# Optimization experiments

Hardware: AMD Instinct MI355X
Metric: run time of the kernel (lower is better)

The kernel has to match this reference:

```python
import jax, jax.numpy as jnp
import numpy as np

D_MODEL, D_K, D_V, H, M = 512, 64, 64, 8, 40
LN_EPS = 1e-3  # keras LayerNormalization default epsilon


def setup_inputs() -> dict:
    key = jax.random.key(0)
    ks = jax.random.split(key, 12)
    b, nq, nk = 16, 1024, 1024
    s = 1.0 / np.sqrt(D_MODEL)
    return {
        "queries": jax.random.normal(ks[0], (b, nq, D_MODEL), jnp.float32),
        "keys": jax.random.normal(ks[1], (b, nk, D_MODEL), jnp.float32),
        "values": jax.random.normal(ks[2], (b, nk, D_MODEL), jnp.float32),
        "attention_weights": jax.random.uniform(ks[3], (b, 1, nq, nk), jnp.float32),
        "Wq": jax.random.normal(ks[4], (D_MODEL, H * D_K), jnp.float32) * s,
        "bq": jnp.zeros((H * D_K,), jnp.float32),
        "Wk": jax.random.normal(ks[5], (D_MODEL, H * D_K), jnp.float32) * s,
        "bk": jnp.zeros((H * D_K,), jnp.float32),
        "Wv": jax.random.normal(ks[6], (D_MODEL, H * D_V), jnp.float32) * s,
        "bv": jnp.zeros((H * D_V,), jnp.float32),
        "Wo": jax.random.normal(ks[7], (H * D_V, D_MODEL), jnp.float32) * (1.0 / np.sqrt(H * D_V)),
        "bo": jnp.zeros((D_MODEL,), jnp.float32),
        "memK": jax.random.normal(ks[8], (1, M, H * D_K), jnp.float32) * (1.0 / D_K),
        "memV": jax.random.normal(ks[9], (1, M, H * D_V), jnp.float32) * (1.0 / M),
        "gamma": jnp.ones((D_MODEL,), jnp.float32),
        "beta": jnp.zeros((D_MODEL,), jnp.float32),
    }


def reference(queries, keys, values, attention_weights, Wq, bq, Wk, bk, Wv, bv,
              Wo, bo, memK, memV, gamma, beta):
    b, nq, _ = queries.shape
    nk = keys.shape[1]
    # scaled learned memory slots
    mem_k = np.sqrt(D_K).astype(np.float32) * memK      # [1, M, H*D_K]
    mem_v = np.sqrt(M).astype(np.float32) * memV        # [1, M, H*D_V]
    # projections
    q = (queries @ Wq + bq).reshape(b, nq, H, D_K).transpose(0, 2, 1, 3)   # [b,h,nq,dk]
    k_proj = keys @ Wk + bk                                                # [b,nk,H*D_K]
    v_proj = values @ Wv + bv                                              # [b,nk,H*D_V]
    k_cat = jnp.concatenate([k_proj, jnp.broadcast_to(mem_k, (b, M, H * D_K))], axis=1)
    v_cat = jnp.concatenate([v_proj, jnp.broadcast_to(mem_v, (b, M, H * D_V))], axis=1)
    k = k_cat.reshape(b, nk + M, H, D_K).transpose(0, 2, 1, 3)             # [b,h,nk+m,dk]
    v = v_cat.reshape(b, nk + M, H, D_V).transpose(0, 2, 1, 3)             # [b,h,nk+m,dv]
    att = jnp.einsum('bhqd,bhkd->bhqk', q, k) / np.sqrt(D_K).astype(np.float32)
    # only the non-memory columns are modulated by attention_weights
    att = jnp.concatenate([att[..., :nk] * attention_weights, att[..., nk:]], axis=-1)
    att = jax.nn.softmax(att, axis=-1)
    out = jnp.einsum('bhqk,bhkd->bhqd', att, v).transpose(0, 2, 1, 3).reshape(b, nq, H * D_V)
    out = out @ Wo + bo  # dropout is identity at inference
    # residual + LayerNorm (keras eps=1e-3)
    x = queries + out
    mu = jnp.mean(x, axis=-1, keepdims=True)
    var = jnp.mean((x - mu) ** 2, axis=-1, keepdims=True)
    return gamma * (x - mu) * jax.lax.rsqrt(var + LN_EPS) + beta
```

## Files before the change

kernel.cpp:

```cpp
#include <hip/hip_runtime.h>
#include <hip/hip_bf16.h>
#include <math.h>

typedef __attribute__((ext_vector_type(8))) short bf16x8;
typedef __attribute__((ext_vector_type(4))) short s16x4;
typedef __attribute__((ext_vector_type(4))) float f32x4;

static __device__ __forceinline__ short f2bf(float f) {
    union { float f; unsigned u; } v; v.f = f;
    unsigned r = v.u + 0x7FFFu + ((v.u >> 16) & 1u);
    return (short)(r >> 16);
}

#define GL2LDS16(g, s) __builtin_amdgcn_global_load_lds( \
    (const __attribute__((address_space(1))) void*)(g),  \
    (__attribute__((address_space(3))) void*)(s), 16, 0, 0)

__global__ __launch_bounds__(256) void wt_kernel(
    const float* __restrict__ Wq, const float* __restrict__ Wk,
    const float* __restrict__ Wv, const float* __restrict__ Wo,
    short* __restrict__ WqT, short* __restrict__ WkT,
    short* __restrict__ WvT, short* __restrict__ WoT)
{
    __shared__ short lds[64][65];
    const float* src; short* dst;
    if (blockIdx.z == 0)      { src = Wq; dst = WqT; }
    else if (blockIdx.z == 1) { src = Wk; dst = WkT; }
    else if (blockIdx.z == 2) { src = Wv; dst = WvT; }
    else                      { src = Wo; dst = WoT; }
    const int kb = blockIdx.x * 64, nb = blockIdx.y * 64;
    const int t = threadIdx.x;
    const int c = t & 63, r0 = t >> 6;
#pragma unroll
    for (int rr = 0; rr < 16; ++rr) {
        const int r = r0 * 16 + rr;
        lds[c][r] = f2bf(src[(size_t)(kb + r) * 512 + nb + c]);
    }
    __syncthreads();
#pragma unroll
    for (int rr = 0; rr < 16; ++rr) {
        const int n = r0 * 16 + rr;
        dst[(size_t)(nb + n) * 512 + kb + c] = lds[n][c];
    }
}

__global__ __launch_bounds__(256) void mem_kernel(
    const float* __restrict__ memK, const float* __restrict__ memV,
    short* __restrict__ Kb, short* __restrict__ VbT)
{
    const int idx = blockIdx.x * 256 + threadIdx.x;
    if (idx >= 16 * 8 * 40 * 64) return;
    const int d = idx & 63;
    const int m = (idx >> 6) % 40;
    const int h = (idx / 2560) & 7;
    const int b = idx / 20480;
    const int src = m * 512 + h * 64 + d;
    const int bh = b * 8 + h;
    Kb[((size_t)bh * 1064 + 1024 + m) * 64 + d] = f2bf(8.0f * memK[src]);
    VbT[((size_t)bh * 64 + d) * 1088 + 1024 + m] = f2bf(sqrtf(40.0f) * memV[src]);
}

__global__ __launch_bounds__(256) void proj_gemm(
    const float* __restrict__ A, const short* __restrict__ BT,
    const float* __restrict__ bias, short* __restrict__ out, int OUTROWS, int vmode)
{
    __shared__ float As[4096];
    __shared__ short Bs[8192];
    const int t = threadIdx.x;
    const int lane = t & 63, w = t >> 6;
    const int wr = w >> 1, wc = w & 1;
    const int l16 = lane & 15, g4 = lane >> 4;
    const int m0 = blockIdx.y * 64, n0 = blockIdx.x * 128;

    f32x4 acc[2][4];
#pragma unroll
    for (int i = 0; i < 2; ++i)
#pragma unroll
        for (int j = 0; j < 4; ++j) acc[i][j] = (f32x4){0.f, 0.f, 0.f, 0.f};

    int arow_[4], acol_[4], brow_[4], bcol_[4];
#pragma unroll
    for (int c = 0; c < 4; ++c) {
        const int chunk = c * 4 + w;
        const int ar = chunk * 4 + (lane >> 4);
        const int alb = ((lane & 15) * 16) ^ ((ar & 7) << 4);
        arow_[c] = ar; acol_[c] = alb >> 2;
        const int br = chunk * 8 + (lane >> 3);
        const int blb = ((lane & 7) * 16) ^ ((br & 7) << 4);
        brow_[c] = br; bcol_[c] = blb >> 1;
    }

    for (int kt = 0; kt < 8; ++kt) {
        const int k0 = kt * 64;
#pragma unroll
        for (int c = 0; c < 4; ++c) {
            GL2LDS16(&A[(size_t)(m0 + arow_[c]) * 512 + k0 + acol_[c]],
                     &As[(c * 4 + w) * 256 + lane * 4]);
            GL2LDS16(&BT[(size_t)(n0 + brow_[c]) * 512 + k0 + bcol_[c]],
                     &Bs[(c * 4 + w) * 512 + lane * 8]);
        }
        __syncthreads();
#pragma unroll
        for (int kk = 0; kk < 2; ++kk) {
            bf16x8 af[2], bfr[4];
#pragma unroll
            for (int mi = 0; mi < 2; ++mi) {
                const int ar = wr * 32 + mi * 16 + l16;
                const int lb0 = (kk * 128 + g4 * 32) ^ ((ar & 7) << 4);
                const float4 f0 = *reinterpret_cast<const float4*>(
                    reinterpret_cast<const char*>(As) + ar * 256 + lb0);
                const float4 f1 = *reinterpret_cast<const float4*>(
                    reinterpret_cast<const char*>(As) + ar * 256 + (lb0 ^ 16));
                bf16x8 a;
                a[0] = f2bf(f0.x); a[1] = f2bf(f0.y); a[2] = f2bf(f0.z); a[3] = f2bf(f0.w);
                a[4] = f2bf(f1.x); a[5] = f2bf(f1.y); a[6] = f2bf(f1.z); a[7] = f2bf(f1.w);
                af[mi] = a;
            }
#pragma unroll
            for (int ni = 0; ni < 4; ++ni) {
                const int br = wc * 64 + ni * 16 + l16;
                const int lb = (kk * 64 + g4 * 16) ^ ((br & 7) << 4);
                bfr[ni] = *reinterpret_cast<const bf16x8*>(
                    reinterpret_cast<const char*>(Bs) + br * 128 + lb);
            }
#pragma unroll
            for (int mi = 0; mi < 2; ++mi)
#pragma unroll
                for (int ni = 0; ni < 4; ++ni)
                    acc[mi][ni] = __builtin_amdgcn_mfma_f32_16x16x32_bf16(af[mi], bfr[ni], acc[mi][ni], 0, 0, 0);
        }
        __syncthreads();
    }
#pragma unroll
    for (int mi = 0; mi < 2; ++mi) {
#pragma unroll
        for (int ni = 0; ni < 4; ++ni) {
            const int col = n0 + wc * 64 + ni * 16 + l16;
            const int h = col >> 6, d = col & 63;
            const float bb = bias[col];
#pragma unroll
            for (int r = 0; r < 4; ++r) {
                const int rowg = m0 + wr * 32 + mi * 16 + g4 * 4 + r;
                const int b = rowg >> 10, nn = rowg & 1023;
                const short val = f2bf(acc[mi][ni][r] + bb);
                if (vmode)
                    out[(((size_t)b * 8 + h) * 64 + d) * 1088 + nn] = val;
                else
                    out[(((size_t)b * 8 + h) * OUTROWS + nn) * 64 + d] = val;
            }
        }
    }
}

__global__ __launch_bounds__(256) void attn_kernel(
    const short* __restrict__ Qb, const short* __restrict__ Kb,
    const short* __restrict__ VbT, const float* __restrict__ aw,
    short* __restrict__ AO)
{
    __shared__ short Ks[64][72];
    __shared__ short Vs[64][72];
    __shared__ short Ps[4][16][72];

    const int n = blockIdx.x;
    const int xcd = n & 7, s_ = n >> 3, j = s_ & 7, gh = s_ >> 3;
    const int g = gh * 8 + xcd;
    const int h = j, qt = g & 15, b = g >> 4;
    const int bh = b * 8 + h;
    const int t = threadIdx.x;
    const int lane = t & 63, w = t >> 6;
    const int l16 = lane & 15, g4 = lane >> 4;
    const int qrow0 = qt * 64 + w * 16;

    bf16x8 qf0, qf1;
    {
        const short* qp = Qb + ((size_t)bh * 1024 + qrow0 + l16) * 64 + g4 * 8;
        qf0 = *reinterpret_cast<const bf16x8*>(qp);
        qf1 = *reinterpret_cast<const bf16x8*>(qp + 32);
    }

    f32x4 O[4];
#pragma unroll
    for (int i = 0; i < 4; ++i) O[i] = (f32x4){0.f, 0.f, 0.f, 0.f};
    float m_r[4] = {-1e30f, -1e30f, -1e30f, -1e30f};
    float l_r[4] = {0.f, 0.f, 0.f, 0.f};

    const int str = t >> 2;
    const int stc = (t & 3) * 16;

    for (int kt = 0; kt < 17; ++kt) {
        const int kb = kt * 64;
        const bool useaw = (kb < 1024);
        float awv[4][4];
        if (useaw) {
#pragma unroll
            for (int r = 0; r < 4; ++r) {
                const size_t awbase = ((size_t)b * 1024 + qrow0 + g4 * 4 + r) * 1024 + kb + l16;
#pragma unroll
                for (int sub = 0; sub < 4; ++sub)
                    awv[r][sub] = aw[awbase + sub * 16];
            }
        }
        {
            const int rg = kb + str;
            bf16x8 k0 = {0,0,0,0,0,0,0,0}, k1 = {0,0,0,0,0,0,0,0};
            if (rg < 1064) {
                const short* kp = &Kb[((size_t)bh * 1064 + rg) * 64 + stc];
                k0 = *reinterpret_cast<const bf16x8*>(kp);
                k1 = *reinterpret_cast<const bf16x8*>(kp + 8);
            }
            *reinterpret_cast<bf16x8*>(&Ks[str][stc]) = k0;
            *reinterpret_cast<bf16x8*>(&Ks[str][stc + 8]) = k1;
        }
        {
            const short* vp = &VbT[((size_t)bh * 64 + str) * 1088 + kb + stc];
            bf16x8 v0 = {0,0,0,0,0,0,0,0}, v1 = {0,0,0,0,0,0,0,0};
            if (kb + stc + 8 <= 1064)  v0 = *reinterpret_cast<const bf16x8*>(vp);
            if (kb + stc + 16 <= 1064) v1 = *reinterpret_cast<const bf16x8*>(vp + 8);
            *reinterpret_cast<bf16x8*>(&Vs[str][stc]) = v0;
            *reinterpret_cast<bf16x8*>(&Vs[str][stc + 8]) = v1;
        }
        __syncthreads();

        f32x4 S[4];
        __builtin_amdgcn_s_setprio(1);
#pragma unroll
        for (int sub = 0; sub < 4; ++sub) {
            bf16x8 kf0 = *reinterpret_cast<const bf16x8*>(&Ks[sub * 16 + l16][g4 * 8]);
            bf16x8 kf1 = *reinterpret_cast<const bf16x8*>(&Ks[sub * 16 + l16][32 + g4 * 8]);
            f32x4 z = {0.f, 0.f, 0.f, 0.f};
            z = __builtin_amdgcn_mfma_f32_16x16x32_bf16(qf0, kf0, z, 0, 0, 0);
            S[sub] = __builtin_amdgcn_mfma_f32_16x16x32_bf16(qf1, kf1, z, 0, 0, 0);
        }
        __builtin_amdgcn_s_setprio(0);

        const bool tail = (kb + 64 > 1064);
        float sv[4][4], mx[4];
#pragma unroll
        for (int r = 0; r < 4; ++r) {
#pragma unroll
            for (int sub = 0; sub < 4; ++sub) {
                float x = S[sub][r] * 0.125f;
                if (useaw) x *= awv[r][sub];
                if (tail && (kb + sub * 16 + l16 >= 1064)) x = -1e30f;
                sv[r][sub] = x;
            }
            float m2 = fmaxf(fmaxf(sv[r][0], sv[r][1]), fmaxf(sv[r][2], sv[r][3]));
#pragma unroll
            for (int off = 1; off < 16; off <<= 1)
                m2 = fmaxf(m2, __shfl_xor(m2, off));
            mx[r] = m2;
        }
        bool grew = false;
#pragma unroll
        for (int r = 0; r < 4; ++r) grew = grew || (mx[r] > m_r[r] + 8.0f);
        if (__any(grew)) {
#pragma unroll
            for (int r = 0; r < 4; ++r) {
                const float mn = fmaxf(m_r[r], mx[r]);
                const float corr = __expf(m_r[r] - mn);
                m_r[r] = mn;
                l_r[r] *= corr;
#pragma unroll
                for (int i = 0; i < 4; ++i) O[i][r] *= corr;
            }
        }
#pragma unroll
        for (int r = 0; r < 4; ++r) {
            float rs = 0.f;
#pragma unroll
            for (int sub = 0; sub < 4; ++sub) {
                const float p = __expf(sv[r][sub] - m_r[r]);
                rs += p;
                Ps[w][g4 * 4 + r][sub * 16 + l16] = f2bf(p);
            }
#pragma unroll
            for (int off = 1; off < 16; off <<= 1)
                rs += __shfl_xor(rs, off);
            l_r[r] += rs;
        }
        bf16x8 pf0 = *reinterpret_cast<const bf16x8*>(&Ps[w][l16][g4 * 8]);
        bf16x8 pf1 = *reinterpret_cast<const bf16x8*>(&Ps[w][l16][32 + g4 * 8]);
        __builtin_amdgcn_s_setprio(1);
#pragma unroll
        for (int sub = 0; sub < 4; ++sub) {
            bf16x8 vf0 = *reinterpret_cast<const bf16x8*>(&Vs[sub * 16 + l16][g4 * 8]);
            bf16x8 vf1 = *reinterpret_cast<const bf16x8*>(&Vs[sub * 16 + l16][32 + g4 * 8]);
            O[sub] = __builtin_amdgcn_mfma_f32_16x16x32_bf16(pf0, vf0, O[sub], 0, 0, 0);
            O[sub] = __builtin_amdgcn_mfma_f32_16x16x32_bf16(pf1, vf1, O[sub], 0, 0, 0);
        }
        __builtin_amdgcn_s_setprio(0);
        __syncthreads();
    }
#pragma unroll
    for (int r = 0; r < 4; ++r) {
        const float inv = 1.0f / l_r[r];
        const int qg = qrow0 + g4 * 4 + r;
        const size_t base = ((size_t)b * 1024 + qg) * 512 + h * 64;
#pragma unroll
        for (int sub = 0; sub < 4; ++sub)
            AO[base + sub * 16 + l16] = f2bf(O[sub][r] * inv);
    }
}

__global__ __launch_bounds__(256) void out_gemm(
    const short* __restrict__ A, const short* __restrict__ BT,
    const float* __restrict__ bias, const float* __restrict__ resid,
    float* __restrict__ out)
{
    __shared__ short Asb[4096];
    __shared__ short Bs[8192];
    const int t = threadIdx.x;
    const int lane = t & 63, w = t >> 6;
    const int wr = w >> 1, wc = w & 1;
    const int l16 = lane & 15, g4 = lane >> 4;
    const int m0 = blockIdx.y * 64, n0 = blockIdx.x * 128;

    f32x4 acc[2][4];
#pragma unroll
    for (int i = 0; i < 2; ++i)
#pragma unroll
        for (int j = 0; j < 4; ++j) acc[i][j] = (f32x4){0.f, 0.f, 0.f, 0.f};

    int arow_[2], acol_[2], brow_[4], bcol_[4];
#pragma unroll
    for (int c = 0; c < 2; ++c) {
        const int chunk = c * 4 + w;
        const int ar = chunk * 8 + (lane >> 3);
        const int alb = ((lane & 7) * 16) ^ ((ar & 7) << 4);
        arow_[c] = ar; acol_[c] = alb >> 1;
    }
#pragma unroll
    for (int c = 0; c < 4; ++c) {
        const int chunk = c * 4 + w;
        const int br = chunk * 8 + (lane >> 3);
        const int blb = ((lane & 7) * 16) ^ ((br & 7) << 4);
        brow_[c] = br; bcol_[c] = blb >> 1;
    }

    for (int kt = 0; kt < 8; ++kt) {
        const int k0 = kt * 64;
#pragma unroll
        for (int c = 0; c < 2; ++c)
            GL2LDS16(&A[(size_t)(m0 + arow_[c]) * 512 + k0 + acol_[c]],
                     &Asb[(c * 4 + w) * 512 + lane * 8]);
#pragma unroll
        for (int c = 0; c < 4; ++c)
            GL2LDS16(&BT[(size_t)(n0 + brow_[c]) * 512 + k0 + bcol_[c]],
                     &Bs[(c * 4 + w) * 512 + lane * 8]);
        __syncthreads();
#pragma unroll
        for (int kk = 0; kk < 2; ++kk) {
            bf16x8 af[2], bfr[4];
#pragma unroll
            for (int mi = 0; mi < 2; ++mi) {
                const int ar = wr * 32 + mi * 16 + l16;
                const int lb = (kk * 64 + g4 * 16) ^ ((ar & 7) << 4);
                af[mi] = *reinterpret_cast<const bf16x8*>(
                    reinterpret_cast<const char*>(Asb) + ar * 128 + lb);
            }
#pragma unroll
            for (int ni = 0; ni < 4; ++ni) {
                const int br = wc * 64 + ni * 16 + l16;
                const int lb = (kk * 64 + g4 * 16) ^ ((br & 7) << 4);
                bfr[ni] = *reinterpret_cast<const bf16x8*>(
                    reinterpret_cast<const char*>(Bs) + br * 128 + lb);
            }
#pragma unroll
            for (int mi = 0; mi < 2; ++mi)
#pragma unroll
                for (int ni = 0; ni < 4; ++ni)
                    acc[mi][ni] = __builtin_amdgcn_mfma_f32_16x16x32_bf16(af[mi], bfr[ni], acc[mi][ni], 0, 0, 0);
        }
        __syncthreads();
    }
#pragma unroll
    for (int mi = 0; mi < 2; ++mi) {
#pragma unroll
        for (int ni = 0; ni < 4; ++ni) {
            const int col = n0 + wc * 64 + ni * 16 + l16;
            const float bb = bias[col];
#pragma unroll
            for (int r = 0; r < 4; ++r) {
                const int rowg = m0 + wr * 32 + mi * 16 + g4 * 4 + r;
                out[(size_t)rowg * 512 + col] = acc[mi][ni][r] + bb + resid[(size_t)rowg * 512 + col];
            }
        }
    }
}

__global__ __launch_bounds__(256) void ln_kernel(
    float* __restrict__ x, const float* __restrict__ gamma, const float* __restrict__ beta)
{
    const int row = blockIdx.x * 4 + (threadIdx.x >> 6);
    const int lane = threadIdx.x & 63;
    float* rp = x + (size_t)row * 512;
    const float4 v0 = *reinterpret_cast<const float4*>(&rp[lane * 4]);
    const float4 v1 = *reinterpret_cast<const float4*>(&rp[256 + lane * 4]);
    float s = v0.x + v0.y + v0.z + v0.w + v1.x + v1.y + v1.z + v1.w;
    float sq = v0.x * v0.x + v0.y * v0.y + v0.z * v0.z + v0.w * v0.w
             + v1.x * v1.x + v1.y * v1.y + v1.z * v1.z + v1.w * v1.w;
#pragma unroll
    for (int off = 1; off < 64; off <<= 1) {
        s += __shfl_xor(s, off);
        sq += __shfl_xor(sq, off);
    }
    const float mu = s * (1.f / 512.f);
    const float var = sq * (1.f / 512.f) - mu * mu;
    const float inv = rsqrtf(var + 1e-3f);
    const float4 g0 = *reinterpret_cast<const float4*>(&gamma[lane * 4]);
    const float4 g1 = *reinterpret_cast<const float4*>(&gamma[256 + lane * 4]);
    const float4 b0 = *reinterpret_cast<const float4*>(&beta[lane * 4]);
    const float4 b1 = *reinterpret_cast<const float4*>(&beta[256 + lane * 4]);
    float4 o0, o1;
    o0.x = (v0.x - mu) * inv * g0.x + b0.x;
    o0.y = (v0.y - mu) * inv * g0.y + b0.y;
    o0.z = (v0.z - mu) * inv * g0.z + b0.z;
    o0.w = (v0.w - mu) * inv * g0.w + b0.w;
    o1.x = (v1.x - mu) * inv * g1.x + b1.x;
    o1.y = (v1.y - mu) * inv * g1.y + b1.y;
    o1.z = (v1.z - mu) * inv * g1.z + b1.z;
    o1.w = (v1.w - mu) * inv * g1.w + b1.w;
    *reinterpret_cast<float4*>(&rp[lane * 4]) = o0;
    *reinterpret_cast<float4*>(&rp[256 + lane * 4]) = o1;
}

extern "C" void kernel_launch(void* const* d_in, const int* in_sizes, int n_in,
                              void* d_out, int out_size, void* d_ws, size_t ws_size,
                              hipStream_t stream) {
    const float* queries = (const float*)d_in[0];
    const float* keys    = (const float*)d_in[1];
    const float* values  = (const float*)d_in[2];
    const float* aw      = (const float*)d_in[3];
    const float* Wq = (const float*)d_in[4];
    const float* bq = (const float*)d_in[5];
    const float* Wk = (const float*)d_in[6];
    const float* bk = (const float*)d_in[7];
    const float* Wv = (const float*)d_in[8];
    const float* bv = (const float*)d_in[9];
    const float* Wo = (const float*)d_in[10];
    const float* bo = (const float*)d_in[11];
    const float* memK = (const float*)d_in[12];
    const float* memV = (const float*)d_in[13];
    const float* gamma = (const float*)d_in[14];
    const float* beta  = (const float*)d_in[15];
    float* out = (float*)d_out;

    char* ws = (char*)d_ws;
    short* WqT = (short*)(ws + 0);
    short* WkT = (short*)(ws + 524288);
    short* WvT = (short*)(ws + 1048576);
    short* WoT = (short*)(ws + 1572864);
    short* Qb  = (short*)(ws + 2097152);
    short* Kb  = (short*)(ws + 2097152 + 16777216);
    short* VbT = (short*)(ws + 2097152 + 16777216 + 17432576);
    short* AO  = (short*)(ws + 2097152 + 16777216 + 17432576 + 17825792);

    wt_kernel<<<dim3(8, 8, 4), 256, 0, stream>>>(Wq, Wk, Wv, Wo, WqT, WkT, WvT, WoT);
    mem_kernel<<<dim3(1280), 256, 0, stream>>>(memK, memV, Kb, VbT);
    proj_gemm<<<dim3(4, 256), 256, 0, stream>>>(queries, WqT, bq, Qb, 1024, 0);
    proj_gemm<<<dim3(4, 256), 256, 0, stream>>>(keys, WkT, bk, Kb, 1064, 0);
    proj_gemm<<<dim3(4, 256), 256, 0, stream>>>(values, WvT, bv, VbT, 1064, 1);
    attn_kernel<<<dim3(2048), 256, 0, stream>>>(Qb, Kb, VbT, aw, AO);
    out_gemm<<<dim3(4, 256), 256, 0, stream>>>(AO, WoT, bo, queries, out);
    ln_kernel<<<dim3(4096), 256, 0, stream>>>(out, gamma, beta);
}
```

Before: 435.6 us.

## Merge Q/K/V projections into one launch with 128x128 tiles and grouped tile order

The three projection GEMMs now run as one launch, with blockIdx.y selecting Q, K or V. Both the projection and output GEMMs grow from 64x128 to 128x128 tiles, raising per-wave MFMA work from 2x4 to 4x4 fragments. Tiles are ordered in groups of eight M-tiles for L2 locality, MFMA sections are raised in priority with s_setprio, and the mem_kernel V-transpose write is reindexed so consecutive threads write contiguous memory. Larger tiles increase register and LDS use (48KB for the proj A/B tiles), which may lower occupancy.

Result: faster. 392.5 us (-9.9%).

```diff
diff --git a/kernel.cpp b/kernel.cpp
--- a/kernel.cpp
+++ b/kernel.cpp
@@ -50,67 +50,85 @@
 {
     const int idx = blockIdx.x * 256 + threadIdx.x;
     if (idx >= 16 * 8 * 40 * 64) return;
-    const int d = idx & 63;
-    const int m = (idx >> 6) % 40;
-    const int h = (idx / 2560) & 7;
-    const int b = idx / 20480;
-    const int src = m * 512 + h * 64 + d;
-    const int bh = b * 8 + h;
-    Kb[((size_t)bh * 1064 + 1024 + m) * 64 + d] = f2bf(8.0f * memK[src]);
-    VbT[((size_t)bh * 64 + d) * 1088 + 1024 + m] = f2bf(sqrtf(40.0f) * memV[src]);
+    {
+        const int d = idx & 63;
+        const int m = (idx >> 6) % 40;
+        const int h = (idx / 2560) & 7;
+        const int b = idx / 20480;
+        Kb[(((size_t)(b * 8 + h)) * 1064 + 1024 + m) * 64 + d] =
+            f2bf(8.0f * memK[m * 512 + h * 64 + d]);
+    }
+    {
+        const int m = idx % 40;
+        const int d = (idx / 40) & 63;
+        const int h = (idx / 2560) & 7;
+        const int b = idx / 20480;
+        VbT[(((size_t)(b * 8 + h)) * 64 + d) * 1088 + 1024 + m] =
+            f2bf(sqrtf(40.0f) * memV[m * 512 + h * 64 + d]);
+    }
 }
 
 __global__ __launch_bounds__(256) void proj_gemm(
-    const float* __restrict__ A, const short* __restrict__ BT,
-    const float* __restrict__ bias, short* __restrict__ out, int OUTROWS, int vmode)
-{
-    __shared__ float As[4096];
-    __shared__ short Bs[8192];
+    const float* __restrict__ Aq, const float* __restrict__ Ak, const float* __restrict__ Av,
+    const short* __restrict__ WqT, const short* __restrict__ WkT, const short* __restrict__ WvT,
+    const float* __restrict__ bq, const float* __restrict__ bk, const float* __restrict__ bv,
+    short* __restrict__ Qb, short* __restrict__ Kb, short* __restrict__ VbT)
+{
+    __shared__ float As[128 * 64];
+    __shared__ short Bs[128 * 64];
+
+    const float* A; const short* BT; const float* bias; short* out;
+    int vmode, OUTROWS;
+    if (blockIdx.y == 0)      { A = Aq; BT = WqT; bias = bq; out = Qb;  vmode = 0; OUTROWS = 1024; }
+    else if (blockIdx.y == 1) { A = Ak; BT = WkT; bias = bk; out = Kb;  vmode = 0; OUTROWS = 1064; }
+    else                      { A = Av; BT = WvT; bias = bv; out = VbT; vmode = 1; OUTROWS = 1064; }
+
+    const int id = blockIdx.x;
+    const int mt = (id & 7) + 8 * (id >> 5);
+    const int nt = (id >> 3) & 3;
+    const int m0 = mt * 128, n0 = nt * 128;
+
     const int t = threadIdx.x;
     const int lane = t & 63, w = t >> 6;
     const int wr = w >> 1, wc = w & 1;
     const int l16 = lane & 15, g4 = lane >> 4;
-    const int m0 = blockIdx.y * 64, n0 = blockIdx.x * 128;
-
-    f32x4 acc[2][4];
-#pragma unroll
-    for (int i = 0; i < 2; ++i)
+
+    f32x4 acc[4][4];
+#pragma unroll
+    for (int i = 0; i < 4; ++i)
 #pragma unroll
         for (int j = 0; j < 4; ++j) acc[i][j] = (f32x4){0.f, 0.f, 0.f, 0.f};
 
-    int arow_[4], acol_[4], brow_[4], bcol_[4];
-#pragma unroll
-    for (int c = 0; c < 4; ++c) {
-        const int chunk = c * 4 + w;
-        const int ar = chunk * 4 + (lane >> 4);
-        const int alb = ((lane & 15) * 16) ^ ((ar & 7) << 4);
-        arow_[c] = ar; acol_[c] = alb >> 2;
-        const int br = chunk * 8 + (lane >> 3);
-        const int blb = ((lane & 7) * 16) ^ ((br & 7) << 4);
-        brow_[c] = br; bcol_[c] = blb >> 1;
-    }
+    const char* Asb = reinterpret_cast<const char*>(As);
+    const char* Bsb = reinterpret_cast<const char*>(Bs);
 
     for (int kt = 0; kt < 8; ++kt) {
         const int k0 = kt * 64;
 #pragma unroll
-        for (int c = 0; c < 4; ++c) {
-            GL2LDS16(&A[(size_t)(m0 + arow_[c]) * 512 + k0 + acol_[c]],
-                     &As[(c * 4 + w) * 256 + lane * 4]);
-            GL2LDS16(&BT[(size_t)(n0 + brow_[c]) * 512 + k0 + bcol_[c]],
-                     &Bs[(c * 4 + w) * 512 + lane * 8]);
+        for (int p = 0; p < 8; ++p) {
+            const int row = p * 16 + (t >> 4);
+            const int ck = (t & 15) ^ (row & 7);
+            GL2LDS16(&A[(size_t)(m0 + row) * 512 + k0 + ck * 4],
+                     (char*)As + (p * 256 + t) * 16);
+        }
+#pragma unroll
+        for (int p = 0; p < 4; ++p) {
+            const int row = p * 32 + (t >> 3);
+            const int ck = (t & 7) ^ (row & 7);
+            GL2LDS16(&BT[(size_t)(n0 + row) * 512 + k0 + ck * 8],
+                     (char*)Bs + (p * 256 + t) * 16);
         }
         __syncthreads();
 #pragma unroll
         for (int kk = 0; kk < 2; ++kk) {
-            bf16x8 af[2], bfr[4];
-#pragma unroll
-            for (int mi = 0; mi < 2; ++mi) {
-                const int ar = wr * 32 + mi * 16 + l16;
-                const int lb0 = (kk * 128 + g4 * 32) ^ ((ar & 7) << 4);
-                const float4 f0 = *reinterpret_cast<const float4*>(
-                    reinterpret_cast<const char*>(As) + ar * 256 + lb0);
-                const float4 f1 = *reinterpret_cast<const float4*>(
-                    reinterpret_cast<const char*>(As) + ar * 256 + (lb0 ^ 16));
+            bf16x8 af[4], bfr[4];
+#pragma unroll
+            for (int mi = 0; mi < 4; ++mi) {
+                const int row = wr * 64 + mi * 16 + l16;
+                const int c0 = (kk * 8 + g4 * 2) ^ (row & 7);
+                const int c1 = (kk * 8 + g4 * 2 + 1) ^ (row & 7);
+                const float4 f0 = *reinterpret_cast<const float4*>(Asb + row * 256 + c0 * 16);
+                const float4 f1 = *reinterpret_cast<const float4*>(Asb + row * 256 + c1 * 16);
                 bf16x8 a;
                 a[0] = f2bf(f0.x); a[1] = f2bf(f0.y); a[2] = f2bf(f0.z); a[3] = f2bf(f0.w);
                 a[4] = f2bf(f1.x); a[5] = f2bf(f1.y); a[6] = f2bf(f1.z); a[7] = f2bf(f1.w);
@@ -118,21 +136,22 @@
             }
 #pragma unroll
             for (int ni = 0; ni < 4; ++ni) {
-                const int br = wc * 64 + ni * 16 + l16;
-                const int lb = (kk * 64 + g4 * 16) ^ ((br & 7) << 4);
-                bfr[ni] = *reinterpret_cast<const bf16x8*>(
-                    reinterpret_cast<const char*>(Bs) + br * 128 + lb);
-            }
-#pragma unroll
-            for (int mi = 0; mi < 2; ++mi)
+                const int row = wc * 64 + ni * 16 + l16;
+                const int ck = (kk * 4 + g4) ^ (row & 7);
+                bfr[ni] = *reinterpret_cast<const bf16x8*>(Bsb + row * 128 + ck * 16);
+            }
+            __builtin_amdgcn_s_setprio(1);
+#pragma unroll
+            for (int mi = 0; mi < 4; ++mi)
 #pragma unroll
                 for (int ni = 0; ni < 4; ++ni)
                     acc[mi][ni] = __builtin_amdgcn_mfma_f32_16x16x32_bf16(af[mi], bfr[ni], acc[mi][ni], 0, 0, 0);
-        }
-        __syncthreads();
-    }
-#pragma unroll
-    for (int mi = 0; mi < 2; ++mi) {
+            __builtin_amdgcn_s_setprio(0);
+        }
+        __syncthreads();
+    }
+#pragma unroll
+    for (int mi = 0; mi < 4; ++mi) {
 #pragma unroll
         for (int ni = 0; ni < 4; ++ni) {
             const int col = n0 + wc * 64 + ni * 16 + l16;
@@ -140,7 +159,7 @@
             const float bb = bias[col];
 #pragma unroll
             for (int r = 0; r < 4; ++r) {
-                const int rowg = m0 + wr * 32 + mi * 16 + g4 * 4 + r;
+                const int rowg = m0 + wr * 64 + mi * 16 + g4 * 4 + r;
                 const int b = rowg >> 10, nn = rowg & 1023;
                 const short val = f2bf(acc[mi][ni][r] + bb);
                 if (vmode)
@@ -307,81 +326,74 @@
     const float* __restrict__ bias, const float* __restrict__ resid,
     float* __restrict__ out)
 {
-    __shared__ short Asb[4096];
-    __shared__ short Bs[8192];
+    __shared__ short Asm[128 * 64];
+    __shared__ short Bs[128 * 64];
+
+    const int id = blockIdx.x;
+    const int mt = (id & 7) + 8 * (id >> 5);
+    const int nt = (id >> 3) & 3;
+    const int m0 = mt * 128, n0 = nt * 128;
+
     const int t = threadIdx.x;
     const int lane = t & 63, w = t >> 6;
     const int wr = w >> 1, wc = w & 1;
     const int l16 = lane & 15, g4 = lane >> 4;
-    const int m0 = blockIdx.y * 64, n0 = blockIdx.x * 128;
-
-    f32x4 acc[2][4];
-#pragma unroll
-    for (int i = 0; i < 2; ++i)
+
+    f32x4 acc[4][4];
+#pragma unroll
+    for (int i = 0; i < 4; ++i)
 #pragma unroll
         for (int j = 0; j < 4; ++j) acc[i][j] = (f32x4){0.f, 0.f, 0.f, 0.f};
 
-    int arow_[2], acol_[2], brow_[4], bcol_[4];
-#pragma unroll
-    for (int c = 0; c < 2; ++c) {
-        const int chunk = c * 4 + w;
-        const int ar = chunk * 8 + (lane >> 3);
-        const int alb = ((lane & 7) * 16) ^ ((ar & 7) << 4);
-        arow_[c] = ar; acol_[c] = alb >> 1;
-    }
-#pragma unroll
-    for (int c = 0; c < 4; ++c) {
-        const int chunk = c * 4 + w;
-        const int br = chunk * 8 + (lane >> 3);
-        const int blb = ((lane & 7) * 16) ^ ((br & 7) << 4);
-        brow_[c] = br; bcol_[c] = blb >> 1;
-    }
+    const char* Asb = reinterpret_cast<const char*>(Asm);
+    const char* Bsb = reinterpret_cast<const char*>(Bs);
 
     for (int kt = 0; kt < 8; ++kt) {
         const int k0 = kt * 64;
 #pragma unroll
-        for (int c = 0; c < 2; ++c)
-            GL2LDS16(&A[(size_t)(m0 + arow_[c]) * 512 + k0 + acol_[c]],
-                     &Asb[(c * 4 + w) * 512 + lane * 8]);
-#pragma unroll
-        for (int c = 0; c < 4; ++c)
-            GL2LDS16(&BT[(size_t)(n0 + brow_[c]) * 512 + k0 + bcol_[c]],
-                     &Bs[(c * 4 + w) * 512 + lane * 8]);
+        for (int p = 0; p < 4; ++p) {
+            const int row = p * 32 + (t >> 3);
+            const int ck = (t & 7) ^ (row & 7);
+            GL2LDS16(&A[(size_t)(m0 + row) * 512 + k0 + ck * 8],
+                     (char*)Asm + (p * 256 + t) * 16);
+            GL2LDS16(&BT[(size_t)(n0 + row) * 512 + k0 + ck * 8],
+                     (char*)Bs + (p * 256 + t) * 16);
+        }
         __syncthreads();
 #pragma unroll
         for (int kk = 0; kk < 2; ++kk) {
-            bf16x8 af[2], bfr[4];
-#pragma unroll
-            for (int mi = 0; mi < 2; ++mi) {
-                const int ar = wr * 32 + mi * 16 + l16;
-                const int lb = (kk * 64 + g4 * 16) ^ ((ar & 7) << 4);
-                af[mi] = *reinterpret_cast<const bf16x8*>(
-                    reinterpret_cast<const char*>(Asb) + ar * 128 + lb);
+            bf16x8 af[4], bfr[4];
+#pragma unroll
+            for (int mi = 0; mi < 4; ++mi) {
+                const int row = wr * 64 + mi * 16 + l16;
+                const int ck = (kk * 4 + g4) ^ (row & 7);
+                af[mi] = *reinterpret_cast<const bf16x8*>(Asb + row * 128 + ck * 16);
             }
 #pragma unroll
             for (int ni = 0; ni < 4; ++ni) {
-                const int br = wc * 64 + ni * 16 + l16;
-                const int lb = (kk * 64 + g4 * 16) ^ ((br & 7) << 4);
-                bfr[ni] = *reinterpret_cast<const bf16x8*>(
-                    reinterpret_cast<const char*>(Bs) + br * 128 + lb);
-            }
-#pragma unroll
-            for (int mi = 0; mi < 2; ++mi)
+                const int row = wc * 64 + ni * 16 + l16;
+                const int ck = (kk * 4 + g4) ^ (row & 7);
+                bfr[ni] = *reinterpret_cast<const bf16x8*>(Bsb + row * 128 + ck * 16);
+            }
+            __builtin_amdgcn_s_setprio(1);
+#pragma unroll
+            for (int mi = 0; mi < 4; ++mi)
 #pragma unroll
                 for (int ni = 0; ni < 4; ++ni)
                     acc[mi][ni] = __builtin_amdgcn_mfma_f32_16x16x32_bf16(af[mi], bfr[ni], acc[mi][ni], 0, 0, 0);
-        }
-        __syncthreads();
-    }
-#pragma unroll
-    for (int mi = 0; mi < 2; ++mi) {
+            __builtin_amdgcn_s_setprio(0);
+        }
+        __syncthreads();
+    }
+#pragma unroll
+    for (int mi = 0; mi < 4; ++mi) {
 #pragma unroll
         for (int ni = 0; ni < 4; ++ni) {
             const int col = n0 + wc * 64 + ni * 16 + l16;
             const float bb = bias[col];
 #pragma unroll
             for (int r = 0; r < 4; ++r) {
-                const int rowg = m0 + wr * 32 + mi * 16 + g4 * 4 + r;
+                const int rowg = m0 + wr * 64 + mi * 16 + g4 * 4 + r;
                 out[(size_t)rowg * 512 + col] = acc[mi][ni][r] + bb + resid[(size_t)rowg * 512 + col];
             }
         }
@@ -457,10 +469,10 @@
 
     wt_kernel<<<dim3(8, 8, 4), 256, 0, stream>>>(Wq, Wk, Wv, Wo, WqT, WkT, WvT, WoT);
     mem_kernel<<<dim3(1280), 256, 0, stream>>>(memK, memV, Kb, VbT);
-    proj_gemm<<<dim3(4, 256), 256, 0, stream>>>(queries, WqT, bq, Qb, 1024, 0);
-    proj_gemm<<<dim3(4, 256), 256, 0, stream>>>(keys, WkT, bk, Kb, 1064, 0);
-    proj_gemm<<<dim3(4, 256), 256, 0, stream>>>(values, WvT, bv, VbT, 1064, 1);
+    proj_gemm<<<dim3(512, 3), 256, 0, stream>>>(queries, keys, values,
+                                                WqT, WkT, WvT, bq, bk, bv,
+                                                Qb, Kb, VbT);
     attn_kernel<<<dim3(2048), 256, 0, stream>>>(Qb, Kb, VbT, aw, AO);
-    out_gemm<<<dim3(4, 256), 256, 0, stream>>>(AO, WoT, bo, queries, out);
+    out_gemm<<<dim3(512), 256, 0, stream>>>(AO, WoT, bo, queries, out);
     ln_kernel<<<dim3(4096), 256, 0, stream>>>(out, gamma, beta);
 }
```
